# Optimization experiments

Measured on AMD Instinct MI355X. Metric: run time of the kernel, lower is better.

The kernel has to match this reference:

```python
import jax, jax.numpy as jnp
import numpy as np

NUM_HEADS = 12

def setup_inputs() -> dict:
    key = jax.random.key(0)
    k1, k2, k3 = jax.random.split(key, 3)
    B, T, S, C = 8, 40, 1024, 768
    N = T + S
    x = jax.random.normal(k1, (B, N, C), dtype=jnp.float32)
    qkv_w = jax.random.normal(k2, (3 * C, C), dtype=jnp.float32) * (C ** -0.5)
    proj_w = jax.random.normal(k3, (C, C), dtype=jnp.float32) * (C ** -0.5)
    proj_b = jnp.zeros((C,), dtype=jnp.float32)
    return {"x": x, "qkv_w": qkv_w, "proj_w": proj_w, "proj_b": proj_b,
            "image_tokens": S, "text_tokens": T}


def reference(x, qkv_w, proj_w, proj_b, image_tokens, text_tokens):
    B, N, C = x.shape
    H = NUM_HEADS
    hd = C // H
    scale = hd ** -0.5
    # qkv: [B,N,3C] -> [3,B,H,N,hd]
    qkv = jnp.einsum('bnc,dc->bnd', x, qkv_w)
    qkv = qkv.reshape(B, N, 3, H, hd).transpose(2, 0, 3, 1, 4)
    q, k, v = qkv[0], qkv[1], qkv[2]
    # text block comes first in the token axis
    q_mt, q_s = q[:, :, :text_tokens], q[:, :, text_tokens:]
    k_mt = k[:, :, :text_tokens]
    v_mt = v[:, :, :text_tokens]
    # text -> text attention
    attn_mt = jax.nn.softmax(jnp.einsum('bhtd,bhsd->bhts', q_mt, k_mt) * scale, axis=-1)
    x_mt = jnp.einsum('bhts,bhsd->bhtd', attn_mt, v_mt)
    x_mt = x_mt.transpose(0, 2, 1, 3).reshape(B, text_tokens, C)
    # image -> all attention
    attn_s = jax.nn.softmax(jnp.einsum('bhid,bhnd->bhin', q_s, k) * scale, axis=-1)
    x_s = jnp.einsum('bhin,bhnd->bhid', attn_s, v)
    x_s = x_s.transpose(0, 2, 1, 3).reshape(B, image_tokens, C)
    out = jnp.concatenate([x_mt, x_s], axis=1)
    out = jnp.einsum('bnc,dc->bnd', out, proj_w) + proj_b
    return out
```

## Files before the change

kernel.cpp:

```cpp
#include <hip/hip_runtime.h>
#include <hip/hip_bf16.h>

typedef __bf16 bf16x8 __attribute__((ext_vector_type(8)));
typedef float f32x4 __attribute__((ext_vector_type(4)));

#define NHEADS 12
#define TT 40
#define ST 1024
#define NTOK 1064
#define CDIM 768
#define HD 64
#define QSCALE 0.18033688f

union U4 {
    uint4 u;
    __hip_bfloat16 h[8];
    bf16x8 v;
};

__device__ __forceinline__ void load_lds16(const __hip_bfloat16* g, __hip_bfloat16* s)
{
    __builtin_amdgcn_global_load_lds(
        (const __attribute__((address_space(1))) void*)g,
        (__attribute__((address_space(3))) void*)s, 16, 0, 0);
}

__global__ __launch_bounds__(256) void f2b3(
    const float* __restrict__ x,  __hip_bfloat16* __restrict__ xo,
    const float* __restrict__ w,  __hip_bfloat16* __restrict__ wo,
    const float* __restrict__ p,  __hip_bfloat16* __restrict__ po)
{
    const float* in; __hip_bfloat16* out; int i;
    if (blockIdx.x < 3192)      { in = x; out = xo; i = blockIdx.x * 256 + threadIdx.x; if (i >= 817152) return; }
    else if (blockIdx.x < 4056) { in = w; out = wo; i = (blockIdx.x - 3192) * 256 + threadIdx.x; if (i >= 221184) return; }
    else                        { in = p; out = po; i = (blockIdx.x - 4056) * 256 + threadIdx.x; if (i >= 73728) return; }
    float4 a = ((const float4*)in)[2 * i];
    float4 b = ((const float4*)in)[2 * i + 1];
    U4 r;
    r.h[0] = __float2bfloat16(a.x); r.h[1] = __float2bfloat16(a.y);
    r.h[2] = __float2bfloat16(a.z); r.h[3] = __float2bfloat16(a.w);
    r.h[4] = __float2bfloat16(b.x); r.h[5] = __float2bfloat16(b.y);
    r.h[6] = __float2bfloat16(b.z); r.h[7] = __float2bfloat16(b.w);
    ((uint4*)out)[i] = r.u;
}

template <int MODE>
__global__ __launch_bounds__(256) void gemm128(
    const __hip_bfloat16* __restrict__ A, int lda, int M,
    const __hip_bfloat16* __restrict__ B, int ldb,
    int K,
    __hip_bfloat16* __restrict__ out0,
    __hip_bfloat16* __restrict__ out1,
    __hip_bfloat16* __restrict__ out2,
    float* __restrict__ outf,
    const float* __restrict__ biasf)
{
    __shared__ __hip_bfloat16 lds[8704];
    __hip_bfloat16* ldsA = lds;
    __hip_bfloat16* ldsB = lds + 128 * 32;

    const int tid = threadIdx.x;
    const int m0 = blockIdx.y * 128;
    const int n0 = blockIdx.x * 128;
    const int w = tid >> 6, l = tid & 63, l15 = l & 15, lq = l >> 4;
    const int wm = w >> 1, wn = w & 1;

    const __hip_bfloat16* srcA[2];
    const __hip_bfloat16* srcB[2];
#pragma unroll
    for (int rd = 0; rd < 2; ++rd) {
        const int c = tid + rd * 256;
        const int r = c >> 2, cs = c & 3;
        const int gs = (cs - (r >> 1)) & 3;
        int ra = m0 + r; if (ra > M - 1) ra = M - 1;
        srcA[rd] = A + (long long)ra * lda + gs * 8;
        srcB[rd] = B + (long long)(n0 + r) * ldb + gs * 8;
    }

    int offA[4], offB[4];
#pragma unroll
    for (int t = 0; t < 4; ++t) {
        { const int r = wm * 64 + t * 16 + l15;
          offA[t] = r * 32 + ((lq + (r >> 1)) & 3) * 8; }
        { const int r = wn * 64 + t * 16 + l15;
          offB[t] = r * 32 + ((lq + (r >> 1)) & 3) * 8; }
    }

    f32x4 acc[4][4] = {};

    const int ksteps = K / 32;
    for (int ks = 0; ks < ksteps; ++ks) {
        __syncthreads();
#pragma unroll
        for (int rd = 0; rd < 2; ++rd) {
            const int c8 = (tid + rd * 256) * 8;
            load_lds16(srcA[rd] + ks * 32, ldsA + c8);
            load_lds16(srcB[rd] + ks * 32, ldsB + c8);
        }
        __syncthreads();

        bf16x8 af[4], bfr[4];
#pragma unroll
        for (int t = 0; t < 4; ++t) af[t] = *(const bf16x8*)(ldsA + offA[t]);
#pragma unroll
        for (int t = 0; t < 4; ++t) bfr[t] = *(const bf16x8*)(ldsB + offB[t]);
#pragma unroll
        for (int tr = 0; tr < 4; ++tr)
#pragma unroll
            for (int tc = 0; tc < 4; ++tc)
                acc[tr][tc] = __builtin_amdgcn_mfma_f32_16x16x32_bf16(af[tr], bfr[tc], acc[tr][tc], 0, 0, 0);
    }

    if (MODE == 0 && n0 >= 1536) {
        __hip_bfloat16* ldsT = lds;
#pragma unroll
        for (int hf = 0; hf < 2; ++hf) {
            __syncthreads();
            if (wn == hf) {
#pragma unroll
                for (int tr = 0; tr < 4; ++tr)
#pragma unroll
                    for (int tc = 0; tc < 4; ++tc) {
                        const int cl = tc * 16 + l15;
                        const int r = wm * 64 + tr * 16 + lq * 4;
                        U4 pk4;
                        pk4.h[0] = __float2bfloat16(acc[tr][tc][0]);
                        pk4.h[1] = __float2bfloat16(acc[tr][tc][1]);
                        pk4.h[2] = __float2bfloat16(acc[tr][tc][2]);
                        pk4.h[3] = __float2bfloat16(acc[tr][tc][3]);
                        *(uint2*)(ldsT + cl * 136 + r) = make_uint2(pk4.u.x, pk4.u.y);
                    }
            }
            __syncthreads();
            const int e = tid >> 2, rseg = (tid & 3) * 32;
            const int hh = (n0 + hf * 64 - 1536) >> 6;
#pragma unroll
            for (int j4 = 0; j4 < 4; ++j4) {
                const int r = rseg + j4 * 8;
                const int row = m0 + r;
                if (row >= 8 * NTOK) continue;
                const int b = row / NTOK;
                const int n = row - b * NTOK;
                __hip_bfloat16* dst = out2 + (((long long)(b * NHEADS + hh)) * HD + e) * NTOK + n;
                if (n + 8 <= NTOK) {
                    *(uint4*)dst = *(const uint4*)(ldsT + e * 136 + r);
                } else {
                    for (int j = 0; j < 8; ++j) {
                        const int row2 = row + j;
                        const int b2 = row2 / NTOK;
                        const int n2 = row2 - b2 * NTOK;
                        out2[(((long long)(b2 * NHEADS + hh)) * HD + e) * NTOK + n2] = ldsT[e * 136 + r + j];
                    }
                }
            }
        }
    } else {
#pragma unroll
        for (int tr = 0; tr < 4; ++tr) {
#pragma unroll
            for (int tc = 0; tc < 4; ++tc) {
                const int col = n0 + wn * 64 + tc * 16 + l15;
#pragma unroll
                for (int i = 0; i < 4; ++i) {
                    const int row = m0 + wm * 64 + tr * 16 + lq * 4 + i;
                    if (row >= M) continue;
                    const float v = acc[tr][tc][i];
                    if (MODE == 0) {
                        const int b = row / NTOK;
                        const int n = row - b * NTOK;
                        const int tq = col / CDIM;
                        const int rem = col - tq * CDIM;
                        const int h = rem >> 6;
                        const int e = rem & 63;
                        const long long gh = (long long)b * NHEADS + h;
                        if (tq == 0) out0[(gh * NTOK + n) * HD + e] = __float2bfloat16(v * QSCALE);
                        else         out1[(gh * NTOK + n) * HD + e] = __float2bfloat16(v);
                    } else {
                        outf[(long long)row * CDIM + col] = v + biasf[col];
                    }
                }
            }
        }
    }
}

__global__ __launch_bounds__(512) void flash_img(
    const __hip_bfloat16* __restrict__ Q,
    const __hip_bfloat16* __restrict__ Kt,
    const __hip_bfloat16* __restrict__ VT,
    __hip_bfloat16* __restrict__ AO)
{
    __shared__ __hip_bfloat16 smem[16384];
    const int gh = blockIdx.x;
    const int qt = blockIdx.y;
    const int tid = threadIdx.x;
    const int w = tid >> 6, l = tid & 63, l15 = l & 15, lq = l >> 4;

    const __hip_bfloat16* Qg = Q + ((long long)gh * NTOK + TT + qt * 128) * HD;
    const __hip_bfloat16* Kg = Kt + (long long)gh * NTOK * HD;
    const __hip_bfloat16* Vg = VT + (long long)gh * HD * NTOK;

    const int r0 = tid >> 3;
    const int g0 = ((tid & 7) - r0) & 7;

    bf16x8 qf[2];
#pragma unroll
    for (int kk = 0; kk < 2; ++kk)
        qf[kk] = *(const bf16x8*)(Qg + (w * 16 + l15) * HD + kk * 32 + lq * 8);

    f32x4 ot[4] = {};
    float lsum = 0.0f;

    load_lds16(Kg + (long long)r0 * HD + g0 * 8, smem + tid * 8);
    load_lds16(Vg + (long long)r0 * NTOK + g0 * 8, smem + 4096 + tid * 8);

    const int segA = ((lq + l15) & 7) * 8;
    const int segB = ((4 + lq + l15) & 7) * 8;
    const int L0 = ((l & 16) ? 32 : 0) + l15;
    const int L1 = L0 + 16;
    const bool hi = (l & 32) != 0;

    for (int kt = 0; kt < 17; ++kt) {
        __syncthreads();

        if (kt < 16) {
            const int np = (kt + 1) * 64;
            __hip_bfloat16* kb = smem + ((kt + 1) & 1) * 8192;
            int kr = np + r0; if (kr > NTOK - 1) kr = NTOK - 1;
            int vc = np + g0 * 8; if (vc > NTOK - 8) vc = NTOK - 8;
            load_lds16(Kg + (long long)kr * HD + g0 * 8, kb + tid * 8);
            load_lds16(Vg + (long long)r0 * NTOK + vc, kb + 4096 + tid * 8);
        }

        const __hip_bfloat16* kbuf = smem + (kt & 1) * 8192;
        const __hip_bfloat16* vbuf = kbuf + 4096;

        f32x4 st[4] = {};
#pragma unroll
        for (int kk = 0; kk < 2; ++kk) {
            const int seg = kk ? segB : segA;
            bf16x8 kf[4];
#pragma unroll
            for (int t = 0; t < 4; ++t)
                kf[t] = *(const bf16x8*)(kbuf + (t * 16 + l15) * 64 + seg);
#pragma unroll
            for (int t = 0; t < 4; ++t)
                st[t] = __builtin_amdgcn_mfma_f32_16x16x32_bf16(kf[t], qf[kk], st[t], 0, 0, 0);
        }

        if (kt == 16) {
#pragma unroll
            for (int t = 0; t < 4; ++t) {
                const int nb = 1024 + t * 16 + lq * 4;
#pragma unroll
                for (int i = 0; i < 4; ++i)
                    if (nb + i >= NTOK) st[t][i] = -1e30f;
            }
        }

        float rs = 0.0f;
#pragma unroll
        for (int t = 0; t < 4; ++t)
#pragma unroll
            for (int i = 0; i < 4; ++i) {
                const float p = exp2f(st[t][i]);
                st[t][i] = p;
                rs += p;
            }
        lsum += rs;

        unsigned pk[4][2];
#pragma unroll
        for (int t = 0; t < 4; ++t)
#pragma unroll
            for (int h = 0; h < 2; ++h) {
                __hip_bfloat162 b2 = __float22bfloat162_rn(
                    make_float2(st[t][2 * h], st[t][2 * h + 1]));
                pk[t][h] = *(unsigned*)&b2;
            }

#pragma unroll
        for (int kk = 0; kk < 2; ++kk) {
            const int seg = kk ? segB : segA;
            bf16x8 vf[4];
#pragma unroll
            for (int te = 0; te < 4; ++te)
                vf[te] = *(const bf16x8*)(vbuf + (te * 16 + l15) * 64 + seg);
            const unsigned a0 = __shfl(pk[2 * kk][0], L0), b0 = __shfl(pk[2 * kk + 1][0], L0);
            const unsigned a1 = __shfl(pk[2 * kk][1], L0), b1 = __shfl(pk[2 * kk + 1][1], L0);
            const unsigned a2 = __shfl(pk[2 * kk][0], L1), b2 = __shfl(pk[2 * kk + 1][0], L1);
            const unsigned a3 = __shfl(pk[2 * kk][1], L1), b3 = __shfl(pk[2 * kk + 1][1], L1);
            union { unsigned u[4]; bf16x8 v; } pu;
            pu.u[0] = hi ? b0 : a0;
            pu.u[1] = hi ? b1 : a1;
            pu.u[2] = hi ? b2 : a2;
            pu.u[3] = hi ? b3 : a3;
#pragma unroll
            for (int te = 0; te < 4; ++te)
                ot[te] = __builtin_amdgcn_mfma_f32_16x16x32_bf16(vf[te], pu.v, ot[te], 0, 0, 0);
        }
    }

    lsum += __shfl_xor(lsum, 16);
    lsum += __shfl_xor(lsum, 32);

    __syncthreads();
    __hip_bfloat16* obuf = smem;
    const float inv = 1.0f / lsum;
#pragma unroll
    for (int te = 0; te < 4; ++te) {
        __hip_bfloat162 x0, x1;
        x0.x = __float2bfloat16(ot[te][0] * inv);
        x0.y = __float2bfloat16(ot[te][1] * inv);
        x1.x = __float2bfloat16(ot[te][2] * inv);
        x1.y = __float2bfloat16(ot[te][3] * inv);
        uint2 u;
        u.x = *(unsigned*)&x0;
        u.y = *(unsigned*)&x1;
        *(uint2*)(obuf + (w * 16 + l15) * 72 + te * 16 + lq * 4) = u;
    }
    __syncthreads();
    {
        const int b = gh / NHEADS, h = gh - b * NHEADS;
        const int r = tid >> 2, cc = (tid & 3) * 16;
        const int token = TT + qt * 128 + r;
        __hip_bfloat16* dst = AO + ((long long)b * NTOK + token) * CDIM + h * HD + cc;
        *(uint4*)dst       = *(const uint4*)(obuf + r * 72 + cc);
        *(uint4*)(dst + 8) = *(const uint4*)(obuf + r * 72 + cc + 8);
    }
}

__global__ __launch_bounds__(256) void text_attn(
    const __hip_bfloat16* __restrict__ Q,
    const __hip_bfloat16* __restrict__ Kt,
    const __hip_bfloat16* __restrict__ VT,
    __hip_bfloat16* __restrict__ AO)
{
    const int gh = blockIdx.x;
    const int b = gh / NHEADS;
    const int h = gh - b * NHEADS;
    __shared__ float smem[3 * 40 * 65];
    float* Qs = smem;
    float* Ks = smem + 40 * 65;
    float* Vs = smem + 2 * 40 * 65;
    const __hip_bfloat16* Qg = Q + (long long)gh * NTOK * HD;
    const __hip_bfloat16* Kg = Kt + (long long)gh * NTOK * HD;
    const __hip_bfloat16* Vg = VT + (long long)gh * HD * NTOK;
    for (int idx = threadIdx.x; idx < 40 * 64; idx += 256) {
        const int n = idx >> 6;
        const int e = idx & 63;
        Qs[n * 65 + e] = __bfloat162float(Qg[n * HD + e]);
        Ks[n * 65 + e] = __bfloat162float(Kg[n * HD + e]);
        Vs[n * 65 + e] = __bfloat162float(Vg[(long long)e * NTOK + n]);
    }
    __syncthreads();
    const int w = threadIdx.x >> 6;
    const int lane = threadIdx.x & 63;
    for (int i = w; i < TT; i += 4) {
        float s = -1e30f;
        if (lane < TT) {
            float a = 0.0f;
            for (int e = 0; e < 64; ++e) a += Qs[i * 65 + e] * Ks[lane * 65 + e];
            s = a;
        }
        float m = s;
        for (int off = 32; off > 0; off >>= 1) m = fmaxf(m, __shfl_xor(m, off));
        float pr = (lane < TT) ? exp2f(s - m) : 0.0f;
        float ssum = pr;
        for (int off = 32; off > 0; off >>= 1) ssum += __shfl_xor(ssum, off);
        pr /= ssum;
        float o = 0.0f;
        for (int j = 0; j < TT; ++j) o += __shfl(pr, j) * Vs[j * 65 + lane];
        AO[((long long)b * NTOK + i) * CDIM + h * HD + lane] = __float2bfloat16(o);
    }
}

extern "C" void kernel_launch(void* const* d_in, const int* in_sizes, int n_in,
                              void* d_out, int out_size, void* d_ws, size_t ws_size,
                              hipStream_t stream)
{
    const float* x      = (const float*)d_in[0];
    const float* qkv_w  = (const float*)d_in[1];
    const float* proj_w = (const float*)d_in[2];
    const float* proj_b = (const float*)d_in[3];
    float* out = (float*)d_out;

    const long long QKV_ELEMS = (long long)8 * NHEADS * NTOK * HD;
    __hip_bfloat16* Q  = (__hip_bfloat16*)d_ws;
    __hip_bfloat16* Kt = Q + QKV_ELEMS;
    __hip_bfloat16* VT = Kt + QKV_ELEMS;
    __hip_bfloat16* AO = VT + QKV_ELEMS;
    __hip_bfloat16* xb = AO;
    __hip_bfloat16* wb = AO + QKV_ELEMS;
    __hip_bfloat16* pb = wb + (long long)3 * CDIM * CDIM;

    f2b3<<<4344, 256, 0, stream>>>(x, xb, qkv_w, wb, proj_w, pb);

    gemm128<0><<<dim3(18, 67), 256, 0, stream>>>(
        xb, CDIM, 8 * NTOK, wb, CDIM, CDIM,
        Q, Kt, VT, nullptr, nullptr);

    text_attn<<<96, 256, 0, stream>>>(Q, Kt, VT, AO);

    flash_img<<<dim3(96, 8), 512, 0, stream>>>(Q, Kt, VT, AO);

    gemm128<3><<<dim3(6, 67), 256, 0, stream>>>(
        AO, CDIM, 8 * NTOK, pb, CDIM, CDIM,
        nullptr, nullptr, nullptr, out, proj_b);
}
```

Baseline: 244.9 us.

## Double-buffer GEMM LDS tiles and fold text attention into flash kernel grid

The bf16 GEMM now uses two LDS buffers. It prefetches the next K-slice with async global-to-LDS loads while the MFMAs run on the current slice, which drops one barrier per K step. Text-to-text attention is moved into extra blocks (qt == 8) of the image flash attention launch, removing the separate text_attn kernel launch and letting both run concurrently. The cost is doubled LDS use in the GEMM, which may lower occupancy, and a divergent branch inside flash_img.

```diff
diff --git a/kernel.cpp b/kernel.cpp
--- a/kernel.cpp
+++ b/kernel.cpp
@@ -55,9 +55,7 @@
     float* __restrict__ outf,
     const float* __restrict__ biasf)
 {
-    __shared__ __hip_bfloat16 lds[8704];
-    __hip_bfloat16* ldsA = lds;
-    __hip_bfloat16* ldsB = lds + 128 * 32;
+    __shared__ __hip_bfloat16 lds[16384];
 
     const int tid = threadIdx.x;
     const int m0 = blockIdx.y * 128;
@@ -67,6 +65,7 @@
 
     const __hip_bfloat16* srcA[2];
     const __hip_bfloat16* srcB[2];
+    int c8[2];
 #pragma unroll
     for (int rd = 0; rd < 2; ++rd) {
         const int c = tid + rd * 256;
@@ -75,6 +74,7 @@
         int ra = m0 + r; if (ra > M - 1) ra = M - 1;
         srcA[rd] = A + (long long)ra * lda + gs * 8;
         srcB[rd] = B + (long long)(n0 + r) * ldb + gs * 8;
+        c8[rd] = c * 8;
     }
 
     int offA[4], offB[4];
@@ -89,21 +89,33 @@
     f32x4 acc[4][4] = {};
 
     const int ksteps = K / 32;
+#pragma unroll
+    for (int rd = 0; rd < 2; ++rd) {
+        load_lds16(srcA[rd], lds + c8[rd]);
+        load_lds16(srcB[rd], lds + 4096 + c8[rd]);
+    }
+
     for (int ks = 0; ks < ksteps; ++ks) {
         __syncthreads();
-#pragma unroll
-        for (int rd = 0; rd < 2; ++rd) {
-            const int c8 = (tid + rd * 256) * 8;
-            load_lds16(srcA[rd] + ks * 32, ldsA + c8);
-            load_lds16(srcB[rd] + ks * 32, ldsB + c8);
-        }
-        __syncthreads();
+
+        if (ks + 1 < ksteps) {
+            const int o = ((ks + 1) & 1) * 8192;
+            const int koff = (ks + 1) * 32;
+#pragma unroll
+            for (int rd = 0; rd < 2; ++rd) {
+                load_lds16(srcA[rd] + koff, lds + o + c8[rd]);
+                load_lds16(srcB[rd] + koff, lds + o + 4096 + c8[rd]);
+            }
+        }
+
+        const __hip_bfloat16* bufA = lds + (ks & 1) * 8192;
+        const __hip_bfloat16* bufB = bufA + 4096;
 
         bf16x8 af[4], bfr[4];
 #pragma unroll
-        for (int t = 0; t < 4; ++t) af[t] = *(const bf16x8*)(ldsA + offA[t]);
-#pragma unroll
-        for (int t = 0; t < 4; ++t) bfr[t] = *(const bf16x8*)(ldsB + offB[t]);
+        for (int t = 0; t < 4; ++t) af[t] = *(const bf16x8*)(bufA + offA[t]);
+#pragma unroll
+        for (int t = 0; t < 4; ++t) bfr[t] = *(const bf16x8*)(bufB + offB[t]);
 #pragma unroll
         for (int tr = 0; tr < 4; ++tr)
 #pragma unroll
@@ -196,9 +208,46 @@
     const int tid = threadIdx.x;
     const int w = tid >> 6, l = tid & 63, l15 = l & 15, lq = l >> 4;
 
-    const __hip_bfloat16* Qg = Q + ((long long)gh * NTOK + TT + qt * 128) * HD;
     const __hip_bfloat16* Kg = Kt + (long long)gh * NTOK * HD;
     const __hip_bfloat16* Vg = VT + (long long)gh * HD * NTOK;
+
+    if (qt == 8) {
+        const int b = gh / NHEADS;
+        const int h = gh - b * NHEADS;
+        float* fs = (float*)smem;
+        float* Qs = fs;
+        float* Ks = fs + 40 * 65;
+        float* Vs = fs + 2 * 40 * 65;
+        const __hip_bfloat16* Qg = Q + (long long)gh * NTOK * HD;
+        for (int idx = tid; idx < 40 * 64; idx += 512) {
+            const int n = idx >> 6;
+            const int e = idx & 63;
+            Qs[n * 65 + e] = __bfloat162float(Qg[n * HD + e]);
+            Ks[n * 65 + e] = __bfloat162float(Kg[n * HD + e]);
+            Vs[n * 65 + e] = __bfloat162float(Vg[(long long)e * NTOK + n]);
+        }
+        __syncthreads();
+        for (int i = w; i < TT; i += 8) {
+            float s = -1e30f;
+            if (l < TT) {
+                float a = 0.0f;
+                for (int e = 0; e < 64; ++e) a += Qs[i * 65 + e] * Ks[l * 65 + e];
+                s = a;
+            }
+            float m = s;
+            for (int off = 32; off > 0; off >>= 1) m = fmaxf(m, __shfl_xor(m, off));
+            float pr = (l < TT) ? exp2f(s - m) : 0.0f;
+            float ssum = pr;
+            for (int off = 32; off > 0; off >>= 1) ssum += __shfl_xor(ssum, off);
+            pr /= ssum;
+            float o = 0.0f;
+            for (int j = 0; j < TT; ++j) o += __shfl(pr, j) * Vs[j * 65 + l];
+            AO[((long long)b * NTOK + i) * CDIM + h * HD + l] = __float2bfloat16(o);
+        }
+        return;
+    }
+
+    const __hip_bfloat16* Qg = Q + ((long long)gh * NTOK + TT + qt * 128) * HD;
 
     const int r0 = tid >> 3;
     const int g0 = ((tid & 7) - r0) & 7;
@@ -330,51 +379,6 @@
     }
 }
 
-__global__ __launch_bounds__(256) void text_attn(
-    const __hip_bfloat16* __restrict__ Q,
-    const __hip_bfloat16* __restrict__ Kt,
-    const __hip_bfloat16* __restrict__ VT,
-    __hip_bfloat16* __restrict__ AO)
-{
-    const int gh = blockIdx.x;
-    const int b = gh / NHEADS;
-    const int h = gh - b * NHEADS;
-    __shared__ float smem[3 * 40 * 65];
-    float* Qs = smem;
-    float* Ks = smem + 40 * 65;
-    float* Vs = smem + 2 * 40 * 65;
-    const __hip_bfloat16* Qg = Q + (long long)gh * NTOK * HD;
-    const __hip_bfloat16* Kg = Kt + (long long)gh * NTOK * HD;
-    const __hip_bfloat16* Vg = VT + (long long)gh * HD * NTOK;
-    for (int idx = threadIdx.x; idx < 40 * 64; idx += 256) {
-        const int n = idx >> 6;
-        const int e = idx & 63;
-        Qs[n * 65 + e] = __bfloat162float(Qg[n * HD + e]);
-        Ks[n * 65 + e] = __bfloat162float(Kg[n * HD + e]);
-        Vs[n * 65 + e] = __bfloat162float(Vg[(long long)e * NTOK + n]);
-    }
-    __syncthreads();
-    const int w = threadIdx.x >> 6;
-    const int lane = threadIdx.x & 63;
-    for (int i = w; i < TT; i += 4) {
-        float s = -1e30f;
-        if (lane < TT) {
-            float a = 0.0f;
-            for (int e = 0; e < 64; ++e) a += Qs[i * 65 + e] * Ks[lane * 65 + e];
-            s = a;
-        }
-        float m = s;
-        for (int off = 32; off > 0; off >>= 1) m = fmaxf(m, __shfl_xor(m, off));
-        float pr = (lane < TT) ? exp2f(s - m) : 0.0f;
-        float ssum = pr;
-        for (int off = 32; off > 0; off >>= 1) ssum += __shfl_xor(ssum, off);
-        pr /= ssum;
-        float o = 0.0f;
-        for (int j = 0; j < TT; ++j) o += __shfl(pr, j) * Vs[j * 65 + lane];
-        AO[((long long)b * NTOK + i) * CDIM + h * HD + lane] = __float2bfloat16(o);
-    }
-}
-
 extern "C" void kernel_launch(void* const* d_in, const int* in_sizes, int n_in,
                               void* d_out, int out_size, void* d_ws, size_t ws_size,
                               hipStream_t stream)
@@ -400,9 +404,7 @@
         xb, CDIM, 8 * NTOK, wb, CDIM, CDIM,
         Q, Kt, VT, nullptr, nullptr);
 
-    text_attn<<<96, 256, 0, stream>>>(Q, Kt, VT, AO);
-
-    flash_img<<<dim3(96, 8), 512, 0, stream>>>(Q, Kt, VT, AO);
+    flash_img<<<dim3(96, 9), 512, 0, stream>>>(Q, Kt, VT, AO);
 
     gemm128<3><<<dim3(6, 67), 256, 0, stream>>>(
         AO, CDIM, 8 * NTOK, pb, CDIM, CDIM,
```

Result: faster. 219.0 us (-10.6%).
